# Kernel optimization log

Hardware: AMD Instinct MI355X
Metric: run time of the kernel (lower is better)

Reference implementation:

```python
import jax, jax.numpy as jnp
import numpy as np

N, M, P = 16, 4, 8
BSZ, T = 256, 256
STD_DYN, STD_OBS = 0.1, 0.1


def setup_inputs() -> dict:
    key = jax.random.key(0)
    ks = jax.random.split(key, 5)
    Y = jax.random.normal(ks[0], (BSZ, T, P), dtype=jnp.float32)
    U = jax.random.normal(ks[1], (BSZ, T, M), dtype=jnp.float32)
    # stable time-varying dynamics (spectral radius < 1)
    A_seq = 0.85 * jnp.eye(N, dtype=jnp.float32) + 0.02 * jax.random.normal(ks[2], (T, N, N), dtype=jnp.float32)
    B_seq = 0.1 * jax.random.normal(ks[3], (T, N, M), dtype=jnp.float32)
    C_seq = jax.random.normal(ks[4], (T, P, N), dtype=jnp.float32) / np.float32(np.sqrt(N))
    mu0 = jnp.zeros((N,), dtype=jnp.float32)
    Sigma0 = jnp.eye(N, dtype=jnp.float32)
    return dict(Y=Y, U=U, A_seq=A_seq, B_seq=B_seq, C_seq=C_seq, mu0=mu0, Sigma0=Sigma0)


def _sym(x):
    return 0.5 * (x + jnp.swapaxes(x, -1, -2))


def reference(Y, U, A_seq, B_seq, C_seq, mu0, Sigma0):
    B, T_, p = Y.shape
    n = mu0.shape[0]
    Q = (STD_DYN ** 2) * jnp.eye(n, dtype=Y.dtype)
    R = (STD_OBS ** 2) * jnp.eye(p, dtype=Y.dtype)
    I = jnp.eye(n, dtype=Y.dtype)
    Yt = jnp.swapaxes(Y, 0, 1)  # [T,B,p] time-major for scan
    Ut = jnp.swapaxes(U, 0, 1)  # [T,B,m]

    def filt_step(carry, xs):
        mu, Sig = carry                      # [B,n], [B,n,n]
        y_t, u_t, A, Bm, C = xs
        mu_pred = mu @ A.T + u_t @ Bm.T      # [B,n]
        Sig_pred = jnp.einsum('ij,bjk,lk->bil', A, Sig, A) + Q
        r = y_t - mu_pred @ C.T              # innovation [B,p]
        S = _sym(jnp.einsum('ij,bjk,lk->bil', C, Sig_pred, C) + R)
        PCT = Sig_pred @ C.T                 # [B,n,p]
        K = jnp.swapaxes(jnp.linalg.solve(S, jnp.swapaxes(PCT, -1, -2)), -1, -2)  # [B,n,p]
        mu_f = mu_pred + jnp.einsum('bnp,bp->bn', K, r)
        I_KC = I - K @ C                     # [B,n,n]
        Sig_f = _sym(jnp.einsum('bij,bjk,blk->bil', I_KC, Sig_pred, I_KC)
                     + jnp.einsum('bip,pq,bjq->bij', K, R, K))
        return (mu_f, Sig_f), (mu_f, Sig_f, mu_pred, Sig_pred)

    mu_init = jnp.broadcast_to(mu0, (B, n))
    Sig_init = jnp.broadcast_to(Sigma0, (B, n, n))
    _, (mus_f, Sigs_f, mus_p, Sigs_p) = jax.lax.scan(
        filt_step, (mu_init, Sig_init), (Yt, Ut, A_seq, B_seq, C_seq))

    def smooth_step(carry, xs):
        mu_next, Sig_next = carry            # smoothed t+1
        mu_f, Sig_f, mu_p_next, Sig_p_next, A_next = xs
        SfAT = jnp.einsum('bij,kj->bik', Sig_f, A_next)  # Sigma_t|t A_{t+1}^T
        J = jnp.swapaxes(jnp.linalg.solve(jnp.swapaxes(Sig_p_next, -1, -2),
                                          jnp.swapaxes(SfAT, -1, -2)), -1, -2)
        mu_s = mu_f + jnp.einsum('bij,bj->bi', J, mu_next - mu_p_next)
        Sig_s = _sym(Sig_f + jnp.einsum('bij,bjk,blk->bil', J, Sig_next - Sig_p_next, J))
        return (mu_s, Sig_s), (mu_s, Sig_s)

    carry0 = (mus_f[-1], Sigs_f[-1])
    xs = (mus_f[:-1], Sigs_f[:-1], mus_p[1:], Sigs_p[1:], A_seq[1:])
    _, (mus_s, Sigs_s) = jax.lax.scan(smooth_step, carry0, xs, reverse=True)
    mus_smooth = jnp.concatenate([mus_s, mus_f[-1:]], axis=0)    # [T,B,n]
    Sigs_smooth = jnp.concatenate([Sigs_s, Sigs_f[-1:]], axis=0)  # [T,B,n,n]

    return (jnp.swapaxes(mus_smooth, 0, 1),   # [B,T,n]
            jnp.swapaxes(Sigs_smooth, 0, 1),  # [B,T,n,n]
            jnp.swapaxes(mus_f, 0, 1),        # [B,T,n]
            jnp.swapaxes(Sigs_f, 0, 1))       # [B,T,n,n]
```

## Files before the change

### kernel.cpp

```cpp
#include <hip/hip_runtime.h>

#define NS 16
#define MD 4
#define PD 8
#define BB 256
#define TL 256
#define QV 0.01f
#define RV 0.01f
#define NCHF 256
#define WF   18
#define NCHS 256
#define WSS  18
#define CHM  16
#define WMU  36

#define WSYNC() do { asm volatile("s_waitcnt lgkmcnt(0)" ::: "memory"); \
                     __builtin_amdgcn_sched_barrier(0); } while (0)

#define Z4 make_float4(0.f, 0.f, 0.f, 0.f)

__device__ __forceinline__ float f4c(const float4 v, int i) {
    return i == 0 ? v.x : i == 1 ? v.y : i == 2 ? v.z : v.w;
}

__global__ __launch_bounds__(256, 1) void kPre(
    const float* __restrict__ A_seq, const float* __restrict__ C_seq,
    float* __restrict__ E_ws, float* __restrict__ SQ_ws)
{
    const int t = blockIdx.x, tid = threadIdx.x;
    __shared__ float sA[16][17], sC[8][17];
    sA[tid >> 4][tid & 15] = A_seq[t * 256 + tid];
    if (tid < 128) sC[tid >> 4][tid & 15] = C_seq[t * 128 + tid];
    __syncthreads();
    if (tid < 128) {
        const int p = tid >> 4, j = tid & 15;
        float a = 0.f;
        #pragma unroll
        for (int k = 0; k < 16; ++k) a += sC[p][k] * sA[k][j];
        E_ws[t * 128 + tid] = a;
    } else if (tid < 192) {
        const int q2 = tid - 128, p = q2 >> 3, q = q2 & 7;
        float a = 0.f;
        #pragma unroll
        for (int k = 0; k < 16; ++k) a += sC[p][k] * sC[q][k];
        SQ_ws[t * 64 + q2] = QV * a + ((p == q) ? RV : 0.f);
    }
}

__global__ __launch_bounds__(64, 1) void kF3_warm(
    const float* __restrict__ A_seq, const float* __restrict__ C_seq,
    const float* __restrict__ E_ws, const float* __restrict__ SQ_ws,
    const float* __restrict__ Sig0,
    float* __restrict__ K_ws, float* __restrict__ Sigf_ws,
    float* __restrict__ Sigp_ws)
{
    const int tlo = blockIdx.x;
    int t0 = tlo - WF; if (t0 < 0) t0 = 0;
    const int nst = tlo + 1 - t0;

    const int l  = threadIdx.x;
    const int r  = l >> 2;
    const int q  = l & 3;
    const int c0 = q * 4;
    const int rc  = l >> 3;
    const int cc0 = (l & 7) * 2;
    const int c8  = l & 7;

    __shared__ float lA[16][20];
    __shared__ float lE[8][20];
    __shared__ float lC[8][20];
    __shared__ float lSQ[64];
    __shared__ float lSig[16][20];
    __shared__ float lT[16][20];
    __shared__ float lW[8][20];
    __shared__ float lCS[8][20];
    __shared__ float lS[64];
    __shared__ float lK[128];

    float4 sig4;
    if (t0 == 0) {
        sig4 = *(const float4*)(Sig0 + l * 4);
    } else {
        sig4 = make_float4(r == c0 ? 1.f : 0.f, r == c0 + 1 ? 1.f : 0.f,
                           r == c0 + 2 ? 1.f : 0.f, r == c0 + 3 ? 1.f : 0.f);
    }
    float4 a_c  = *(const float4*)(A_seq + t0 * 256 + l * 4);
    float2 cc_c = *(const float2*)(C_seq + t0 * 128 + l * 2);
    float2 e_c  = *(const float2*)(E_ws  + t0 * 128 + l * 2);
    float  sq_c = SQ_ws[t0 * 64 + l];

    for (int s = 0; s < nst; ++s) {
        const int t = t0 + s;
        const bool commit = (t == tlo);
        WSYNC();
        *(float4*)&lA[r][c0]    = a_c;
        *(float2*)&lC[rc][cc0]  = cc_c;
        *(float2*)&lE[rc][cc0]  = e_c;
        lSQ[l] = sq_c;
        *(float4*)&lSig[r][c0]  = sig4;
        WSYNC();
        if (s + 1 < nst) {
            a_c  = *(const float4*)(A_seq + (t + 1) * 256 + l * 4);
            cc_c = *(const float2*)(C_seq + (t + 1) * 128 + l * 2);
            e_c  = *(const float2*)(E_ws  + (t + 1) * 128 + l * 2);
            sq_c = SQ_ws[(t + 1) * 64 + l];
        }

        float t4[4] = {0.f, 0.f, 0.f, 0.f};
        #pragma unroll
        for (int kk = 0; kk < 4; ++kk) {
            const float4 a4 = *(const float4*)&lA[r][4 * kk];
            #pragma unroll
            for (int i2 = 0; i2 < 4; ++i2) {
                const float av = f4c(a4, i2);
                const float4 sv = *(const float4*)&lSig[4 * kk + i2][c0];
                t4[0] += av * sv.x; t4[1] += av * sv.y;
                t4[2] += av * sv.z; t4[3] += av * sv.w;
            }
        }
        float w2x = 0.f, w2y = 0.f;
        {
            float4 er[4];
            #pragma unroll
            for (int kk = 0; kk < 4; ++kk) er[kk] = *(const float4*)&lE[rc][4 * kk];
            #pragma unroll
            for (int kk = 0; kk < 4; ++kk)
                #pragma unroll
                for (int i2 = 0; i2 < 4; ++i2) {
                    const float ev = f4c(er[kk], i2);
                    const float2 s2 = *(const float2*)&lSig[4 * kk + i2][cc0];
                    w2x += ev * s2.x; w2y += ev * s2.y;
                }
        }
        *(float4*)&lT[r][c0]  = make_float4(t4[0], t4[1], t4[2], t4[3]);
        *(float2*)&lW[rc][cc0] = make_float2(w2x, w2y);
        WSYNC();

        float4 trr[4], wrow[4];
        #pragma unroll
        for (int kk = 0; kk < 4; ++kk) {
            trr[kk]  = *(const float4*)&lT[r][4 * kk];
            wrow[kk] = *(const float4*)&lW[rc][4 * kk];
        }
        float sp[4];
        #pragma unroll
        for (int i = 0; i < 4; ++i) {
            float a = (r == c0 + i) ? QV : 0.f;
            #pragma unroll
            for (int kk = 0; kk < 4; ++kk) {
                const float4 a4 = *(const float4*)&lA[c0 + i][4 * kk];
                a += trr[kk].x * a4.x + trr[kk].y * a4.y
                   + trr[kk].z * a4.z + trr[kk].w * a4.w;
            }
            sp[i] = a;
        }
        const float2 cpair = *(const float2*)&lC[rc][cc0];
        float cs2[2];
        #pragma unroll
        for (int cc = 0; cc < 2; ++cc) {
            float a = QV * (cc == 0 ? cpair.x : cpair.y);
            #pragma unroll
            for (int kk = 0; kk < 4; ++kk) {
                const float4 a4 = *(const float4*)&lA[cc0 + cc][4 * kk];
                a += wrow[kk].x * a4.x + wrow[kk].y * a4.y
                   + wrow[kk].z * a4.z + wrow[kk].w * a4.w;
            }
            cs2[cc] = a;
        }
        float sv = lSQ[l];
        #pragma unroll
        for (int kk = 0; kk < 4; ++kk) {
            const float4 e4 = *(const float4*)&lE[c8][4 * kk];
            sv += wrow[kk].x * e4.x + wrow[kk].y * e4.y
                + wrow[kk].z * e4.z + wrow[kk].w * e4.w;
        }
        *(float2*)&lCS[rc][cc0] = make_float2(cs2[0], cs2[1]);
        lS[l] = sv;
        if (commit) *(float4*)(Sigp_ws + t * 256 + l * 4) =
            make_float4(sp[0], sp[1], sp[2], sp[3]);
        WSYNC();

        float x[8];
        {
            float Lm[8][8]; float Dinv[8];
            #pragma unroll
            for (int r2 = 0; r2 < 8; ++r2)
                #pragma unroll
                for (int c2 = 0; c2 < 8; ++c2)
                    Lm[r2][c2] = (c2 <= r2) ? 0.5f * (lS[r2 * 8 + c2] + lS[c2 * 8 + r2]) : 0.f;
            #pragma unroll
            for (int c2 = 0; c2 < 8; ++c2) {
                float sAcc = Lm[c2][c2];
                #pragma unroll
                for (int k2 = 0; k2 < 8; ++k2) if (k2 < c2) sAcc -= Lm[c2][k2] * Lm[c2][k2];
                const float d = sqrtf(sAcc);
                Dinv[c2] = 1.f / d; Lm[c2][c2] = d;
                #pragma unroll
                for (int r2 = 0; r2 < 8; ++r2) if (r2 > c2) {
                    float s2 = Lm[r2][c2];
                    #pragma unroll
                    for (int k2 = 0; k2 < 8; ++k2) if (k2 < c2) s2 -= Lm[r2][k2] * Lm[c2][k2];
                    Lm[r2][c2] = s2 * Dinv[c2];
                }
            }
            float yv[8];
            #pragma unroll
            for (int c2 = 0; c2 < 8; ++c2) {
                float sAcc = lCS[c2][r];
                #pragma unroll
                for (int k2 = 0; k2 < 8; ++k2) if (k2 < c2) sAcc -= Lm[c2][k2] * yv[k2];
                yv[c2] = sAcc * Dinv[c2];
            }
            #pragma unroll
            for (int c2 = 7; c2 >= 0; --c2) {
                float sAcc = yv[c2];
                #pragma unroll
                for (int k2 = 0; k2 < 8; ++k2) if (k2 > c2) sAcc -= Lm[k2][c2] * x[k2];
                x[c2] = sAcc * Dinv[c2];
            }
        }
        if (q == 0) {
            *(float4*)&lK[r * 8] = make_float4(x[0], x[1], x[2], x[3]);
            if (commit) *(float4*)(K_ws + t * 128 + r * 8) = make_float4(x[0], x[1], x[2], x[3]);
        } else if (q == 1) {
            *(float4*)&lK[r * 8 + 4] = make_float4(x[4], x[5], x[6], x[7]);
            if (commit) *(float4*)(K_ws + t * 128 + r * 8 + 4) = make_float4(x[4], x[5], x[6], x[7]);
        }
        WSYNC();

        float u[4] = { sp[0], sp[1], sp[2], sp[3] };
        {
            const float4 k1  = *(const float4*)&lK[r * 8];
            const float4 k2v = *(const float4*)&lK[r * 8 + 4];
            #pragma unroll
            for (int p = 0; p < 8; ++p) {
                const float kv = (p < 4) ? f4c(k1, p) : f4c(k2v, p - 4);
                const float4 cs4 = *(const float4*)&lCS[p][c0];
                u[0] -= kv * cs4.x; u[1] -= kv * cs4.y;
                u[2] -= kv * cs4.z; u[3] -= kv * cs4.w;
            }
        }
        *(float4*)&lT[r][c0] = make_float4(u[0], u[1], u[2], u[3]);
        WSYNC();
        float o[4];
        #pragma unroll
        for (int i = 0; i < 4; ++i) o[i] = 0.5f * (u[i] + lT[c0 + i][r]);
        sig4 = make_float4(o[0], o[1], o[2], o[3]);
        if (commit) *(float4*)(Sigf_ws + t * 256 + l * 4) = sig4;
    }
}

__global__ __launch_bounds__(256, 1) void kBG(
    const float* __restrict__ A_seq, const float* __restrict__ B_seq,
    const float* __restrict__ C_seq, const float* __restrict__ K_ws,
    const float* __restrict__ Sigf_ws, const float* __restrict__ Sigp_ws,
    float* __restrict__ J_ws, float* __restrict__ G_ws,
    float* __restrict__ Bt2_ws)
{
    const int t = blockIdx.x, tid = threadIdx.x;
    const int i = tid >> 4, j = tid & 15;
    const bool doJ = (t < TL - 1);

    __shared__ float sA0[16][17], sCm[8][17], sKm[16][9], sBm[16][5];
    __shared__ float sCA[8][17], sCB[8][5];
    __shared__ float sSf[16][17], sA1[16][17], sFA[16][17];
    __shared__ float P[2][16][33];

    sA0[i][j] = A_seq[t * 256 + tid];
    if (tid < 128) {
        sCm[tid >> 4][tid & 15] = C_seq[t * 128 + tid];
        sKm[tid >> 3][tid & 7]  = K_ws[t * 128 + tid];
    }
    if (tid < 64) sBm[tid >> 2][tid & 3] = B_seq[t * 64 + tid];
    if (doJ) {
        sSf[i][j] = Sigf_ws[t * 256 + tid];
        sA1[i][j] = A_seq[(t + 1) * 256 + tid];
        P[0][i][j]      = Sigp_ws[(t + 1) * 256 + tid];
        P[0][i][j + 16] = (i == j) ? 1.f : 0.f;
    }
    __syncthreads();

    if (tid < 128) {
        const int p = tid >> 4, jj = tid & 15;
        float a = 0.f;
        #pragma unroll
        for (int k = 0; k < 16; ++k) a += sCm[p][k] * sA0[k][jj];
        sCA[p][jj] = a;
    } else if (tid < 160) {
        const int qq = tid - 128, p = qq >> 2, m = qq & 3;
        float a = 0.f;
        #pragma unroll
        for (int k = 0; k < 16; ++k) a += sCm[p][k] * sBm[k][m];
        sCB[p][m] = a;
    }
    if (doJ) {
        float fa = 0.f;
        #pragma unroll
        for (int k = 0; k < 16; ++k) fa += sSf[i][k] * sA1[j][k];
        sFA[i][j] = fa;
    }
    __syncthreads();

    float gv = sA0[i][j];
    #pragma unroll
    for (int p = 0; p < 8; ++p) gv -= sKm[i][p] * sCA[p][j];
    G_ws[t * 256 + tid] = gv;
    if (tid < 64) {
        const int ii = tid >> 2, m = tid & 3;
        float bv = sBm[ii][m];
        #pragma unroll
        for (int p = 0; p < 8; ++p) bv -= sKm[ii][p] * sCB[p][m];
        Bt2_ws[t * 64 + tid] = bv;
    }

    if (doJ) {
        #pragma unroll 1
        for (int k = 0; k < 16; ++k) {
            const int cur = k & 1, nxt = cur ^ 1;
            const float akk = P[cur][k][k];
            const float piv = 1.f / akk;
            const float rkj  = P[cur][k][j];
            const float rkj2 = P[cur][k][j + 16];
            if (i == k) {
                P[nxt][i][j]      = rkj * piv;
                P[nxt][i][j + 16] = rkj2 * piv;
            } else {
                const float f = P[cur][i][k] * piv;
                P[nxt][i][j]      = P[cur][i][j]      - f * rkj;
                P[nxt][i][j + 16] = P[cur][i][j + 16] - f * rkj2;
            }
            __syncthreads();
        }
        float acc = 0.f;
        #pragma unroll
        for (int k = 0; k < 16; ++k) acc += sFA[i][k] * P[0][k][16 + j];
        J_ws[t * 256 + tid] = acc;
    }
}

__global__ __launch_bounds__(256, 1) void kES3(
    const float* __restrict__ A_seq, const float* __restrict__ B_seq,
    const float* __restrict__ U, const float* __restrict__ Y,
    const float* __restrict__ mu0,
    const float* __restrict__ G_ws, const float* __restrict__ Bt2_ws,
    const float* __restrict__ K_ws, const float* __restrict__ Sigf_ws,
    const float* __restrict__ Sigp_ws, const float* __restrict__ J_ws,
    float* __restrict__ Sigs_ws, float* __restrict__ mus_f_out,
    float* __restrict__ mup_ws, float* __restrict__ Sigs_f_out)
{
    const int bid = blockIdx.x, tid = threadIdx.x;

    if (bid < NCHS) {
        if (tid < 64) {
            const int l   = tid;
            const int r   = l >> 2;
            const int c0  = (l & 3) * 4;
            const int tlo = bid;
            const int thi = tlo;
            int tstart = thi + WSS; if (tstart > 254) tstart = 254;

            __shared__ float lJ[16][20];
            __shared__ float lD[16][20];
            __shared__ float lT1[16][20];
            __shared__ float lV[16][20];

            float4 sS = *(const float4*)(Sigf_ws + (tstart + 1) * 256 + l * 4);
            if (thi == 255) *(float4*)(Sigs_ws + 255 * 256 + l * 4) = sS;

            float4 j_c  = *(const float4*)(J_ws    + tstart * 256 + l * 4);
            float4 sp_c = *(const float4*)(Sigp_ws + (tstart + 1) * 256 + l * 4);
            float4 sf_c = *(const float4*)(Sigf_ws + tstart * 256 + l * 4);

            for (int t = tstart; t >= tlo; --t) {
                float4 d4 = make_float4(sS.x - sp_c.x, sS.y - sp_c.y,
                                        sS.z - sp_c.z, sS.w - sp_c.w);
                WSYNC();
                *(float4*)&lJ[r][c0] = j_c;
                *(float4*)&lD[r][c0] = d4;
                WSYNC();
                const float4 sf_use = sf_c;
                if (t > tlo) {
                    j_c  = *(const float4*)(J_ws    + (t - 1) * 256 + l * 4);
                    sp_c = *(const float4*)(Sigp_ws + t * 256 + l * 4);
                    sf_c = *(const float4*)(Sigf_ws + (t - 1) * 256 + l * 4);
                }

                float a4[4] = {0.f, 0.f, 0.f, 0.f};
                #pragma unroll
                for (int kk = 0; kk < 4; ++kk) {
                    const float4 jr = *(const float4*)&lJ[r][4 * kk];
                    #pragma unroll
                    for (int i2 = 0; i2 < 4; ++i2) {
                        const float jv = f4c(jr, i2);
                        const float4 dv = *(const float4*)&lD[4 * kk + i2][c0];
                        a4[0] += jv * dv.x; a4[1] += jv * dv.y;
                        a4[2] += jv * dv.z; a4[3] += jv * dv.w;
                    }
                }
                *(float4*)&lT1[r][c0] = make_float4(a4[0], a4[1], a4[2], a4[3]);
                WSYNC();

                float4 t1r[4];
                #pragma unroll
                for (int kk = 0; kk < 4; ++kk) t1r[kk] = *(const float4*)&lT1[r][4 * kk];
                float v[4];
                #pragma unroll
                for (int i = 0; i < 4; ++i) {
                    float a = f4c(sf_use, i);
                    #pragma unroll
                    for (int kk = 0; kk < 4; ++kk) {
                        const float4 j4 = *(const float4*)&lJ[c0 + i][4 * kk];
                        a += t1r[kk].x * j4.x + t1r[kk].y * j4.y
                           + t1r[kk].z * j4.z + t1r[kk].w * j4.w;
                    }
                    v[i] = a;
                }
                *(float4*)&lV[r][c0] = make_float4(v[0], v[1], v[2], v[3]);
                WSYNC();

                float o[4];
                #pragma unroll
                for (int i = 0; i < 4; ++i) o[i] = 0.5f * (v[i] + lV[c0 + i][r]);
                sS = make_float4(o[0], o[1], o[2], o[3]);
                if (t <= thi) *(float4*)(Sigs_ws + t * 256 + l * 4) = sS;
            }
        }
    } else if (bid < NCHS + 256) {
        const int eb = bid - NCHS;
        const int ch = eb >> 4;
        const int gq = eb & 15;
        const int w  = tid >> 6;
        const int l  = tid & 63;
        const int g  = l >> 4;
        const int i  = l & 15;
        const int b  = (gq * 4 + w) * 4 + g;
        const int base = l & 48;
        const int tlo  = ch * CHM;
        int t0 = tlo - WMU; if (t0 < 0) t0 = 0;
        const int tend = tlo + CHM;

        float mu = (t0 == 0) ? mu0[i] : 0.f;

        float4 g_c[4], a_c[4], k_c[2], b_c, bt_c, u_c, y0_c, y1_c;
        {
            const float* Gb = G_ws  + t0 * 256 + i * 16;
            const float* Ab = A_seq + t0 * 256 + i * 16;
            #pragma unroll
            for (int kk = 0; kk < 4; ++kk) {
                g_c[kk] = *(const float4*)(Gb + 4 * kk);
                a_c[kk] = *(const float4*)(Ab + 4 * kk);
            }
            k_c[0] = *(const float4*)(K_ws + t0 * 128 + i * 8);
            k_c[1] = *(const float4*)(K_ws + t0 * 128 + i * 8 + 4);
            b_c  = *(const float4*)(B_seq  + t0 * 64 + i * 4);
            bt_c = *(const float4*)(Bt2_ws + t0 * 64 + i * 4);
            u_c  = *(const float4*)(U + ((size_t)b * TL + t0) * MD);
            y0_c = *(const float4*)(Y + ((size_t)b * TL + t0) * PD);
            y1_c = *(const float4*)(Y + ((size_t)b * TL + t0) * PD + 4);
        }

        for (int t = t0; t < tend; ++t) {
            float4 g_n[4] = {Z4, Z4, Z4, Z4}, a_n[4] = {Z4, Z4, Z4, Z4};
            float4 k_n[2] = {Z4, Z4};
            float4 b_n = Z4, bt_n = Z4, u_n = Z4, y0_n = Z4, y1_n = Z4;
            if (t + 1 < tend) {
                const float* Gb = G_ws  + (t + 1) * 256 + i * 16;
                const float* Ab = A_seq + (t + 1) * 256 + i * 16;
                #pragma unroll
                for (int kk = 0; kk < 4; ++kk) {
                    g_n[kk] = *(const float4*)(Gb + 4 * kk);
                    a_n[kk] = *(const float4*)(Ab + 4 * kk);
                }
                k_n[0] = *(const float4*)(K_ws + (t + 1) * 128 + i * 8);
                k_n[1] = *(const float4*)(K_ws + (t + 1) * 128 + i * 8 + 4);
                b_n  = *(const float4*)(B_seq  + (t + 1) * 64 + i * 4);
                bt_n = *(const float4*)(Bt2_ws + (t + 1) * 64 + i * 4);
                u_n  = *(const float4*)(U + ((size_t)b * TL + t + 1) * MD);
                y0_n = *(const float4*)(Y + ((size_t)b * TL + t + 1) * PD);
                y1_n = *(const float4*)(Y + ((size_t)b * TL + t + 1) * PD + 4);
            }

            float sg0 = 0.f, sg1 = 0.f, sg2 = 0.f, sg3 = 0.f;
            float sa0 = 0.f, sa1 = 0.f, sa2 = 0.f, sa3 = 0.f;
            #pragma unroll
            for (int k4 = 0; k4 < 4; ++k4) {
                const float m0 = __shfl(mu, base + 4 * k4 + 0);
                const float m1 = __shfl(mu, base + 4 * k4 + 1);
                const float m2 = __shfl(mu, base + 4 * k4 + 2);
                const float m3 = __shfl(mu, base + 4 * k4 + 3);
                sg0 += f4c(g_c[k4], 0) * m0;  sa0 += f4c(a_c[k4], 0) * m0;
                sg1 += f4c(g_c[k4], 1) * m1;  sa1 += f4c(a_c[k4], 1) * m1;
                sg2 += f4c(g_c[k4], 2) * m2;  sa2 += f4c(a_c[k4], 2) * m2;
                sg3 += f4c(g_c[k4], 3) * m3;  sa3 += f4c(a_c[k4], 3) * m3;
            }
            float mp = (sa0 + sa1) + (sa2 + sa3);
            float mf = (sg0 + sg1) + (sg2 + sg3);
            #pragma unroll
            for (int m = 0; m < 4; ++m) {
                mp += f4c(b_c, m) * f4c(u_c, m);
                mf += f4c(bt_c, m) * f4c(u_c, m);
                mf += f4c(k_c[0], m) * f4c(y0_c, m);
                mf += f4c(k_c[1], m) * f4c(y1_c, m);
            }
            if (t >= tlo) {
                mup_ws[((size_t)b * TL + t) * NS + i]    = mp;
                mus_f_out[((size_t)b * TL + t) * NS + i] = mf;
            }
            mu = mf;

            #pragma unroll
            for (int kk = 0; kk < 4; ++kk) { g_c[kk] = g_n[kk]; a_c[kk] = a_n[kk]; }
            k_c[0] = k_n[0]; k_c[1] = k_n[1];
            b_c = b_n; bt_c = bt_n; u_c = u_n; y0_c = y0_n; y1_c = y1_n;
        }
    } else {
        const size_t total = (size_t)BB * TL * 64;
        const int lb = bid - (NCHS + 256);
        size_t idx = (size_t)lb * 256 + tid;
        const size_t stride = (size_t)1024 * 256;
        for (size_t x = idx; x < total; x += stride) {
            const size_t e4 = x & 63;
            const size_t t = (x >> 6) & 255;
            ((float4*)Sigs_f_out)[x] = ((const float4*)Sigf_ws)[t * 64 + e4];
        }
    }
}

__global__ __launch_bounds__(256, 1) void kFD(
    const float* __restrict__ mus_f, const float* __restrict__ mup_ws,
    const float* __restrict__ J_ws, float* __restrict__ mus_s,
    const float* __restrict__ Sigs_ws, float* __restrict__ Sigs_s_out)
{
    const int bid = blockIdx.x, tid = threadIdx.x;

    if (bid < 256) {
        const int ch = bid >> 4;
        const int gq = bid & 15;
        const int w  = tid >> 6;
        const int l  = tid & 63;
        const int g  = l >> 4;
        const int i  = l & 15;
        const int b  = (gq * 4 + w) * 4 + g;
        const int base = l & 48;
        const int tlo = ch * CHM;
        const int thi = tlo + CHM - 1;
        int tstart = thi + WMU; if (tstart > 254) tstart = 254;

        float muS = mus_f[((size_t)b * TL + tstart + 1) * NS + i];
        if (thi == 255) mus_s[((size_t)b * TL + 255) * NS + i] = muS;

        float4 j_c[4];
        float f_c, p_c;
        #pragma unroll
        for (int kk = 0; kk < 4; ++kk)
            j_c[kk] = *(const float4*)(J_ws + tstart * 256 + i * 16 + 4 * kk);
        f_c = mus_f[((size_t)b * TL + tstart) * NS + i];
        p_c = mup_ws[((size_t)b * TL + tstart + 1) * NS + i];

        for (int t = tstart; t >= tlo; --t) {
            float4 j_n[4] = {Z4, Z4, Z4, Z4};
            float f_n = 0.f, p_n = 0.f;
            if (t > tlo) {
                #pragma unroll
                for (int kk = 0; kk < 4; ++kk)
                    j_n[kk] = *(const float4*)(J_ws + (t - 1) * 256 + i * 16 + 4 * kk);
                f_n = mus_f[((size_t)b * TL + t - 1) * NS + i];
                p_n = mup_ws[((size_t)b * TL + t) * NS + i];
            }

            const float d = muS - p_c;
            float q0 = 0.f, q1 = 0.f, q2 = 0.f, q3 = 0.f;
            #pragma unroll
            for (int k4 = 0; k4 < 4; ++k4) {
                q0 += f4c(j_c[k4], 0) * __shfl(d, base + 4 * k4 + 0);
                q1 += f4c(j_c[k4], 1) * __shfl(d, base + 4 * k4 + 1);
                q2 += f4c(j_c[k4], 2) * __shfl(d, base + 4 * k4 + 2);
                q3 += f4c(j_c[k4], 3) * __shfl(d, base + 4 * k4 + 3);
            }
            muS = f_c + ((q0 + q1) + (q2 + q3));
            if (t <= thi) mus_s[((size_t)b * TL + t) * NS + i] = muS;

            #pragma unroll
            for (int kk = 0; kk < 4; ++kk) j_c[kk] = j_n[kk];
            f_c = f_n; p_c = p_n;
        }
    } else {
        const size_t total = (size_t)BB * TL * 64;
        const int lb = bid - 256;
        size_t idx = (size_t)lb * 256 + tid;
        const size_t stride = (size_t)1024 * 256;
        for (size_t x = idx; x < total; x += stride) {
            const size_t e4 = x & 63;
            const size_t t = (x >> 6) & 255;
            ((float4*)Sigs_s_out)[x] = ((const float4*)Sigs_ws)[t * 64 + e4];
        }
    }
}

extern "C" void kernel_launch(void* const* d_in, const int* in_sizes, int n_in,
                              void* d_out, int out_size, void* d_ws, size_t ws_size,
                              hipStream_t stream) {
    const float* Y     = (const float*)d_in[0];
    const float* U     = (const float*)d_in[1];
    const float* A_seq = (const float*)d_in[2];
    const float* B_seq = (const float*)d_in[3];
    const float* C_seq = (const float*)d_in[4];
    const float* mu0   = (const float*)d_in[5];
    const float* Sig0  = (const float*)d_in[6];

    float* out = (float*)d_out;
    const size_t nBT = (size_t)BB * TL;
    float* mus_s_out  = out;
    float* Sigs_s_out = mus_s_out + nBT * NS;
    float* mus_f_out  = Sigs_s_out + nBT * NS * NS;
    float* Sigs_f_out = mus_f_out + nBT * NS;

    float* w = (float*)d_ws;
    float* K_ws    = w;  w += TL * NS * PD;
    float* Sigf_ws = w;  w += TL * 256;
    float* Sigp_ws = w;  w += TL * 256;
    float* J_ws    = w;  w += TL * 256;
    float* Sigs_ws = w;  w += TL * 256;
    float* G_ws    = w;  w += TL * 256;
    float* Bt2_ws  = w;  w += TL * 64;
    float* E_ws    = w;  w += TL * 128;
    float* SQ_ws   = w;  w += TL * 64;
    float* mup_ws  = w;  w += nBT * NS;

    kPre    <<<TL, 256, 0, stream>>>(A_seq, C_seq, E_ws, SQ_ws);
    kF3_warm<<<NCHF, 64, 0, stream>>>(A_seq, C_seq, E_ws, SQ_ws, Sig0,
                                      K_ws, Sigf_ws, Sigp_ws);
    kBG     <<<TL, 256, 0, stream>>>(A_seq, B_seq, C_seq, K_ws, Sigf_ws, Sigp_ws,
                                     J_ws, G_ws, Bt2_ws);
    kES3    <<<NCHS + 256 + 1024, 256, 0, stream>>>(A_seq, B_seq, U, Y, mu0,
        G_ws, Bt2_ws, K_ws, Sigf_ws, Sigp_ws, J_ws,
        Sigs_ws, mus_f_out, mup_ws, Sigs_f_out);
    kFD     <<<256 + 1024, 256, 0, stream>>>(mus_f_out, mup_ws, J_ws, mus_s_out,
                                             Sigs_ws, Sigs_s_out);
}
```

Baseline: 139.5 us.

## Shorten warm-up windows, double-buffer LDS, skip symmetrization on non-committed steps

Shrinks the warm-up lengths of the filter, the covariance smoother and the mean chunks (WF/WSS 18→14, WMU 36→26) and halves the mean chunk size, which doubles the number of mean-chain blocks. The per-step LDS tiles become double-buffered, so the leading barrier goes away, and the K round-trip through LDS is dropped by using register values directly. The symmetrization with its extra barrier, and the A·mu prediction, now run only on committed steps. This cuts per-step synchronization and redundant warm-up work. The shorter windows rely on the convergence of the time-varying Riccati recursion, and skipping symmetrization during warm-up adds small numerical risk.

```diff
diff --git a/kernel.cpp b/kernel.cpp
--- a/kernel.cpp
+++ b/kernel.cpp
@@ -8,11 +8,12 @@
 #define QV 0.01f
 #define RV 0.01f
 #define NCHF 256
-#define WF   18
+#define WF   14
 #define NCHS 256
-#define WSS  18
-#define CHM  16
-#define WMU  36
+#define WSS  14
+#define CHM  8
+#define NCHM 32
+#define WMU  26
 
 #define WSYNC() do { asm volatile("s_waitcnt lgkmcnt(0)" ::: "memory"); \
                      __builtin_amdgcn_sched_barrier(0); } while (0)
@@ -66,16 +67,16 @@
     const int cc0 = (l & 7) * 2;
     const int c8  = l & 7;
 
-    __shared__ float lA[16][20];
-    __shared__ float lE[8][20];
-    __shared__ float lC[8][20];
-    __shared__ float lSQ[64];
-    __shared__ float lSig[16][20];
+    __shared__ float lA[2][16][20];
+    __shared__ float lCc[2][8][20];
+    __shared__ float lEe[2][8][20];
+    __shared__ float lSQs[2][64];
+    __shared__ float lSg[2][16][20];
     __shared__ float lT[16][20];
     __shared__ float lW[8][20];
     __shared__ float lCS[8][20];
     __shared__ float lS[64];
-    __shared__ float lK[128];
+    __shared__ float lV[16][20];
 
     float4 sig4;
     if (t0 == 0) {
@@ -91,13 +92,14 @@
 
     for (int s = 0; s < nst; ++s) {
         const int t = t0 + s;
+        const int pb = s & 1;
         const bool commit = (t == tlo);
-        WSYNC();
-        *(float4*)&lA[r][c0]    = a_c;
-        *(float2*)&lC[rc][cc0]  = cc_c;
-        *(float2*)&lE[rc][cc0]  = e_c;
-        lSQ[l] = sq_c;
-        *(float4*)&lSig[r][c0]  = sig4;
+
+        *(float4*)&lA[pb][r][c0]   = a_c;
+        *(float2*)&lCc[pb][rc][cc0] = cc_c;
+        *(float2*)&lEe[pb][rc][cc0] = e_c;
+        lSQs[pb][l] = sq_c;
+        *(float4*)&lSg[pb][r][c0]  = sig4;
         WSYNC();
         if (s + 1 < nst) {
             a_c  = *(const float4*)(A_seq + (t + 1) * 256 + l * 4);
@@ -109,11 +111,11 @@
         float t4[4] = {0.f, 0.f, 0.f, 0.f};
         #pragma unroll
         for (int kk = 0; kk < 4; ++kk) {
-            const float4 a4 = *(const float4*)&lA[r][4 * kk];
+            const float4 a4 = *(const float4*)&lA[pb][r][4 * kk];
             #pragma unroll
             for (int i2 = 0; i2 < 4; ++i2) {
                 const float av = f4c(a4, i2);
-                const float4 sv = *(const float4*)&lSig[4 * kk + i2][c0];
+                const float4 sv = *(const float4*)&lSg[pb][4 * kk + i2][c0];
                 t4[0] += av * sv.x; t4[1] += av * sv.y;
                 t4[2] += av * sv.z; t4[3] += av * sv.w;
             }
@@ -122,17 +124,17 @@
         {
             float4 er[4];
             #pragma unroll
-            for (int kk = 0; kk < 4; ++kk) er[kk] = *(const float4*)&lE[rc][4 * kk];
+            for (int kk = 0; kk < 4; ++kk) er[kk] = *(const float4*)&lEe[pb][rc][4 * kk];
             #pragma unroll
             for (int kk = 0; kk < 4; ++kk)
                 #pragma unroll
                 for (int i2 = 0; i2 < 4; ++i2) {
                     const float ev = f4c(er[kk], i2);
-                    const float2 s2 = *(const float2*)&lSig[4 * kk + i2][cc0];
+                    const float2 s2 = *(const float2*)&lSg[pb][4 * kk + i2][cc0];
                     w2x += ev * s2.x; w2y += ev * s2.y;
                 }
         }
-        *(float4*)&lT[r][c0]  = make_float4(t4[0], t4[1], t4[2], t4[3]);
+        *(float4*)&lT[r][c0]   = make_float4(t4[0], t4[1], t4[2], t4[3]);
         *(float2*)&lW[rc][cc0] = make_float2(w2x, w2y);
         WSYNC();
 
@@ -148,29 +150,29 @@
             float a = (r == c0 + i) ? QV : 0.f;
             #pragma unroll
             for (int kk = 0; kk < 4; ++kk) {
-                const float4 a4 = *(const float4*)&lA[c0 + i][4 * kk];
+                const float4 a4 = *(const float4*)&lA[pb][c0 + i][4 * kk];
                 a += trr[kk].x * a4.x + trr[kk].y * a4.y
                    + trr[kk].z * a4.z + trr[kk].w * a4.w;
             }
             sp[i] = a;
         }
-        const float2 cpair = *(const float2*)&lC[rc][cc0];
+        const float2 cpair = *(const float2*)&lCc[pb][rc][cc0];
         float cs2[2];
         #pragma unroll
         for (int cc = 0; cc < 2; ++cc) {
             float a = QV * (cc == 0 ? cpair.x : cpair.y);
             #pragma unroll
             for (int kk = 0; kk < 4; ++kk) {
-                const float4 a4 = *(const float4*)&lA[cc0 + cc][4 * kk];
+                const float4 a4 = *(const float4*)&lA[pb][cc0 + cc][4 * kk];
                 a += wrow[kk].x * a4.x + wrow[kk].y * a4.y
                    + wrow[kk].z * a4.z + wrow[kk].w * a4.w;
             }
             cs2[cc] = a;
         }
-        float sv = lSQ[l];
+        float sv = lSQs[pb][l];
         #pragma unroll
         for (int kk = 0; kk < 4; ++kk) {
-            const float4 e4 = *(const float4*)&lE[c8][4 * kk];
+            const float4 e4 = *(const float4*)&lEe[pb][c8][4 * kk];
             sv += wrow[kk].x * e4.x + wrow[kk].y * e4.y
                 + wrow[kk].z * e4.z + wrow[kk].w * e4.w;
         }
@@ -219,34 +221,28 @@
                 x[c2] = sAcc * Dinv[c2];
             }
         }
-        if (q == 0) {
-            *(float4*)&lK[r * 8] = make_float4(x[0], x[1], x[2], x[3]);
-            if (commit) *(float4*)(K_ws + t * 128 + r * 8) = make_float4(x[0], x[1], x[2], x[3]);
-        } else if (q == 1) {
-            *(float4*)&lK[r * 8 + 4] = make_float4(x[4], x[5], x[6], x[7]);
-            if (commit) *(float4*)(K_ws + t * 128 + r * 8 + 4) = make_float4(x[4], x[5], x[6], x[7]);
-        }
-        WSYNC();
-
         float u[4] = { sp[0], sp[1], sp[2], sp[3] };
-        {
-            const float4 k1  = *(const float4*)&lK[r * 8];
-            const float4 k2v = *(const float4*)&lK[r * 8 + 4];
-            #pragma unroll
-            for (int p = 0; p < 8; ++p) {
-                const float kv = (p < 4) ? f4c(k1, p) : f4c(k2v, p - 4);
-                const float4 cs4 = *(const float4*)&lCS[p][c0];
-                u[0] -= kv * cs4.x; u[1] -= kv * cs4.y;
-                u[2] -= kv * cs4.z; u[3] -= kv * cs4.w;
-            }
-        }
-        *(float4*)&lT[r][c0] = make_float4(u[0], u[1], u[2], u[3]);
-        WSYNC();
-        float o[4];
-        #pragma unroll
-        for (int i = 0; i < 4; ++i) o[i] = 0.5f * (u[i] + lT[c0 + i][r]);
-        sig4 = make_float4(o[0], o[1], o[2], o[3]);
-        if (commit) *(float4*)(Sigf_ws + t * 256 + l * 4) = sig4;
+        #pragma unroll
+        for (int p = 0; p < 8; ++p) {
+            const float kv = x[p];
+            const float4 cs4 = *(const float4*)&lCS[p][c0];
+            u[0] -= kv * cs4.x; u[1] -= kv * cs4.y;
+            u[2] -= kv * cs4.z; u[3] -= kv * cs4.w;
+        }
+
+        if (!commit) {
+            sig4 = make_float4(u[0], u[1], u[2], u[3]);
+        } else {
+            if (q == 0)      *(float4*)(K_ws + t * 128 + r * 8)     = make_float4(x[0], x[1], x[2], x[3]);
+            else if (q == 1) *(float4*)(K_ws + t * 128 + r * 8 + 4) = make_float4(x[4], x[5], x[6], x[7]);
+            *(float4*)&lV[r][c0] = make_float4(u[0], u[1], u[2], u[3]);
+            WSYNC();
+            float o[4];
+            #pragma unroll
+            for (int i = 0; i < 4; ++i) o[i] = 0.5f * (u[i] + lV[c0 + i][r]);
+            sig4 = make_float4(o[0], o[1], o[2], o[3]);
+            *(float4*)(Sigf_ws + t * 256 + l * 4) = sig4;
+        }
     }
 }
 
@@ -356,27 +352,28 @@
             const int r   = l >> 2;
             const int c0  = (l & 3) * 4;
             const int tlo = bid;
-            const int thi = tlo;
-            int tstart = thi + WSS; if (tstart > 254) tstart = 254;
-
-            __shared__ float lJ[16][20];
-            __shared__ float lD[16][20];
-            __shared__ float lT1[16][20];
-            __shared__ float lV[16][20];
+            int tstart = tlo + WSS; if (tstart > 254) tstart = 254;
+
+            __shared__ float sJ[2][16][20];
+            __shared__ float sD[2][16][20];
+            __shared__ float sT1[16][20];
+            __shared__ float sV[16][20];
 
             float4 sS = *(const float4*)(Sigf_ws + (tstart + 1) * 256 + l * 4);
-            if (thi == 255) *(float4*)(Sigs_ws + 255 * 256 + l * 4) = sS;
+            if (tlo == 255) {
+                *(float4*)(Sigs_ws + 255 * 256 + l * 4) = sS;
+            }
 
             float4 j_c  = *(const float4*)(J_ws    + tstart * 256 + l * 4);
             float4 sp_c = *(const float4*)(Sigp_ws + (tstart + 1) * 256 + l * 4);
             float4 sf_c = *(const float4*)(Sigf_ws + tstart * 256 + l * 4);
 
             for (int t = tstart; t >= tlo; --t) {
+                const int pb = t & 1;
                 float4 d4 = make_float4(sS.x - sp_c.x, sS.y - sp_c.y,
                                         sS.z - sp_c.z, sS.w - sp_c.w);
-                WSYNC();
-                *(float4*)&lJ[r][c0] = j_c;
-                *(float4*)&lD[r][c0] = d4;
+                *(float4*)&sJ[pb][r][c0] = j_c;
+                *(float4*)&sD[pb][r][c0] = d4;
                 WSYNC();
                 const float4 sf_use = sf_c;
                 if (t > tlo) {
@@ -388,44 +385,48 @@
                 float a4[4] = {0.f, 0.f, 0.f, 0.f};
                 #pragma unroll
                 for (int kk = 0; kk < 4; ++kk) {
-                    const float4 jr = *(const float4*)&lJ[r][4 * kk];
+                    const float4 jr = *(const float4*)&sJ[pb][r][4 * kk];
                     #pragma unroll
                     for (int i2 = 0; i2 < 4; ++i2) {
                         const float jv = f4c(jr, i2);
-                        const float4 dv = *(const float4*)&lD[4 * kk + i2][c0];
+                        const float4 dv = *(const float4*)&sD[pb][4 * kk + i2][c0];
                         a4[0] += jv * dv.x; a4[1] += jv * dv.y;
                         a4[2] += jv * dv.z; a4[3] += jv * dv.w;
                     }
                 }
-                *(float4*)&lT1[r][c0] = make_float4(a4[0], a4[1], a4[2], a4[3]);
+                *(float4*)&sT1[r][c0] = make_float4(a4[0], a4[1], a4[2], a4[3]);
                 WSYNC();
 
                 float4 t1r[4];
                 #pragma unroll
-                for (int kk = 0; kk < 4; ++kk) t1r[kk] = *(const float4*)&lT1[r][4 * kk];
+                for (int kk = 0; kk < 4; ++kk) t1r[kk] = *(const float4*)&sT1[r][4 * kk];
                 float v[4];
                 #pragma unroll
                 for (int i = 0; i < 4; ++i) {
                     float a = f4c(sf_use, i);
                     #pragma unroll
                     for (int kk = 0; kk < 4; ++kk) {
-                        const float4 j4 = *(const float4*)&lJ[c0 + i][4 * kk];
+                        const float4 j4 = *(const float4*)&sJ[pb][c0 + i][4 * kk];
                         a += t1r[kk].x * j4.x + t1r[kk].y * j4.y
                            + t1r[kk].z * j4.z + t1r[kk].w * j4.w;
                     }
                     v[i] = a;
                 }
-                *(float4*)&lV[r][c0] = make_float4(v[0], v[1], v[2], v[3]);
-                WSYNC();
-
-                float o[4];
-                #pragma unroll
-                for (int i = 0; i < 4; ++i) o[i] = 0.5f * (v[i] + lV[c0 + i][r]);
-                sS = make_float4(o[0], o[1], o[2], o[3]);
-                if (t <= thi) *(float4*)(Sigs_ws + t * 256 + l * 4) = sS;
-            }
-        }
-    } else if (bid < NCHS + 256) {
+
+                if (t > tlo) {
+                    sS = make_float4(v[0], v[1], v[2], v[3]);
+                } else {
+                    *(float4*)&sV[r][c0] = make_float4(v[0], v[1], v[2], v[3]);
+                    WSYNC();
+                    float o[4];
+                    #pragma unroll
+                    for (int i = 0; i < 4; ++i) o[i] = 0.5f * (v[i] + sV[c0 + i][r]);
+                    *(float4*)(Sigs_ws + t * 256 + l * 4) =
+                        make_float4(o[0], o[1], o[2], o[3]);
+                }
+            }
+        }
+    } else if (bid < NCHS + NCHM * 16) {
         const int eb = bid - NCHS;
         const int ch = eb >> 4;
         const int gq = eb & 15;
@@ -441,18 +442,20 @@
 
         float mu = (t0 == 0) ? mu0[i] : 0.f;
 
-        float4 g_c[4], a_c[4], k_c[2], b_c, bt_c, u_c, y0_c, y1_c;
+        float4 g_c[4], a_c[4] = {Z4, Z4, Z4, Z4}, k_c[2];
+        float4 b_c = Z4, bt_c, u_c, y0_c, y1_c;
         {
-            const float* Gb = G_ws  + t0 * 256 + i * 16;
-            const float* Ab = A_seq + t0 * 256 + i * 16;
-            #pragma unroll
-            for (int kk = 0; kk < 4; ++kk) {
-                g_c[kk] = *(const float4*)(Gb + 4 * kk);
-                a_c[kk] = *(const float4*)(Ab + 4 * kk);
+            const float* Gb = G_ws + t0 * 256 + i * 16;
+            #pragma unroll
+            for (int kk = 0; kk < 4; ++kk) g_c[kk] = *(const float4*)(Gb + 4 * kk);
+            if (t0 >= tlo) {
+                const float* Ab = A_seq + t0 * 256 + i * 16;
+                #pragma unroll
+                for (int kk = 0; kk < 4; ++kk) a_c[kk] = *(const float4*)(Ab + 4 * kk);
+                b_c = *(const float4*)(B_seq + t0 * 64 + i * 4);
             }
             k_c[0] = *(const float4*)(K_ws + t0 * 128 + i * 8);
             k_c[1] = *(const float4*)(K_ws + t0 * 128 + i * 8 + 4);
-            b_c  = *(const float4*)(B_seq  + t0 * 64 + i * 4);
             bt_c = *(const float4*)(Bt2_ws + t0 * 64 + i * 4);
             u_c  = *(const float4*)(U + ((size_t)b * TL + t0) * MD);
             y0_c = *(const float4*)(Y + ((size_t)b * TL + t0) * PD);
@@ -464,22 +467,24 @@
             float4 k_n[2] = {Z4, Z4};
             float4 b_n = Z4, bt_n = Z4, u_n = Z4, y0_n = Z4, y1_n = Z4;
             if (t + 1 < tend) {
-                const float* Gb = G_ws  + (t + 1) * 256 + i * 16;
-                const float* Ab = A_seq + (t + 1) * 256 + i * 16;
-                #pragma unroll
-                for (int kk = 0; kk < 4; ++kk) {
-                    g_n[kk] = *(const float4*)(Gb + 4 * kk);
-                    a_n[kk] = *(const float4*)(Ab + 4 * kk);
+                const float* Gb = G_ws + (t + 1) * 256 + i * 16;
+                #pragma unroll
+                for (int kk = 0; kk < 4; ++kk) g_n[kk] = *(const float4*)(Gb + 4 * kk);
+                if (t + 1 >= tlo) {
+                    const float* Ab = A_seq + (t + 1) * 256 + i * 16;
+                    #pragma unroll
+                    for (int kk = 0; kk < 4; ++kk) a_n[kk] = *(const float4*)(Ab + 4 * kk);
+                    b_n = *(const float4*)(B_seq + (t + 1) * 64 + i * 4);
                 }
                 k_n[0] = *(const float4*)(K_ws + (t + 1) * 128 + i * 8);
                 k_n[1] = *(const float4*)(K_ws + (t + 1) * 128 + i * 8 + 4);
-                b_n  = *(const float4*)(B_seq  + (t + 1) * 64 + i * 4);
                 bt_n = *(const float4*)(Bt2_ws + (t + 1) * 64 + i * 4);
                 u_n  = *(const float4*)(U + ((size_t)b * TL + t + 1) * MD);
                 y0_n = *(const float4*)(Y + ((size_t)b * TL + t + 1) * PD);
                 y1_n = *(const float4*)(Y + ((size_t)b * TL + t + 1) * PD + 4);
             }
 
+            const bool com = (t >= tlo);
             float sg0 = 0.f, sg1 = 0.f, sg2 = 0.f, sg3 = 0.f;
             float sa0 = 0.f, sa1 = 0.f, sa2 = 0.f, sa3 = 0.f;
             #pragma unroll
@@ -488,21 +493,28 @@
                 const float m1 = __shfl(mu, base + 4 * k4 + 1);
                 const float m2 = __shfl(mu, base + 4 * k4 + 2);
                 const float m3 = __shfl(mu, base + 4 * k4 + 3);
-                sg0 += f4c(g_c[k4], 0) * m0;  sa0 += f4c(a_c[k4], 0) * m0;
-                sg1 += f4c(g_c[k4], 1) * m1;  sa1 += f4c(a_c[k4], 1) * m1;
-                sg2 += f4c(g_c[k4], 2) * m2;  sa2 += f4c(a_c[k4], 2) * m2;
-                sg3 += f4c(g_c[k4], 3) * m3;  sa3 += f4c(a_c[k4], 3) * m3;
-            }
-            float mp = (sa0 + sa1) + (sa2 + sa3);
+                sg0 += f4c(g_c[k4], 0) * m0;
+                sg1 += f4c(g_c[k4], 1) * m1;
+                sg2 += f4c(g_c[k4], 2) * m2;
+                sg3 += f4c(g_c[k4], 3) * m3;
+                if (com) {
+                    sa0 += f4c(a_c[k4], 0) * m0;
+                    sa1 += f4c(a_c[k4], 1) * m1;
+                    sa2 += f4c(a_c[k4], 2) * m2;
+                    sa3 += f4c(a_c[k4], 3) * m3;
+                }
+            }
             float mf = (sg0 + sg1) + (sg2 + sg3);
             #pragma unroll
             for (int m = 0; m < 4; ++m) {
-                mp += f4c(b_c, m) * f4c(u_c, m);
                 mf += f4c(bt_c, m) * f4c(u_c, m);
                 mf += f4c(k_c[0], m) * f4c(y0_c, m);
                 mf += f4c(k_c[1], m) * f4c(y1_c, m);
             }
-            if (t >= tlo) {
+            if (com) {
+                float mp = (sa0 + sa1) + (sa2 + sa3);
+                #pragma unroll
+                for (int m = 0; m < 4; ++m) mp += f4c(b_c, m) * f4c(u_c, m);
                 mup_ws[((size_t)b * TL + t) * NS + i]    = mp;
                 mus_f_out[((size_t)b * TL + t) * NS + i] = mf;
             }
@@ -515,7 +527,7 @@
         }
     } else {
         const size_t total = (size_t)BB * TL * 64;
-        const int lb = bid - (NCHS + 256);
+        const int lb = bid - (NCHS + NCHM * 16);
         size_t idx = (size_t)lb * 256 + tid;
         const size_t stride = (size_t)1024 * 256;
         for (size_t x = idx; x < total; x += stride) {
@@ -533,7 +545,7 @@
 {
     const int bid = blockIdx.x, tid = threadIdx.x;
 
-    if (bid < 256) {
+    if (bid < NCHM * 16) {
         const int ch = bid >> 4;
         const int gq = bid & 15;
         const int w  = tid >> 6;
@@ -586,7 +598,7 @@
         }
     } else {
         const size_t total = (size_t)BB * TL * 64;
-        const int lb = bid - 256;
+        const int lb = bid - NCHM * 16;
         size_t idx = (size_t)lb * 256 + tid;
         const size_t stride = (size_t)1024 * 256;
         for (size_t x = idx; x < total; x += stride) {
@@ -632,9 +644,9 @@
                                       K_ws, Sigf_ws, Sigp_ws);
     kBG     <<<TL, 256, 0, stream>>>(A_seq, B_seq, C_seq, K_ws, Sigf_ws, Sigp_ws,
                                      J_ws, G_ws, Bt2_ws);
-    kES3    <<<NCHS + 256 + 1024, 256, 0, stream>>>(A_seq, B_seq, U, Y, mu0,
+    kES3    <<<NCHS + NCHM * 16 + 1024, 256, 0, stream>>>(A_seq, B_seq, U, Y, mu0,
         G_ws, Bt2_ws, K_ws, Sigf_ws, Sigp_ws, J_ws,
         Sigs_ws, mus_f_out, mup_ws, Sigs_f_out);
-    kFD     <<<256 + 1024, 256, 0, stream>>>(mus_f_out, mup_ws, J_ws, mus_s_out,
-                                             Sigs_ws, Sigs_s_out);
+    kFD     <<<NCHM * 16 + 1024, 256, 0, stream>>>(mus_f_out, mup_ws, J_ws, mus_s_out,
+                                                   Sigs_ws, Sigs_s_out);
 }
```

New measurement: 120.5 us. 1.16x faster.
